# Kernel tuning notes

Hardware: AMD Instinct MI355X
Metric: run time of the kernel (lower is better)

## Reference

```python
import jax, jax.numpy as jnp
import numpy as np
from jax.ops import segment_sum, segment_max

N, E, F, H, G, P, C = 50000, 600000, 128, 128, 64, 32, 10
HEADS = 3
BN_EPS = 1e-5
COS_EPS = 1e-8


def setup_inputs() -> dict:
    key = jax.random.key(0)
    ks = jax.random.split(key, 32)
    rn = lambda k, shape, s: jax.random.normal(k, shape, jnp.float32) * s
    inp = {
        "x": jax.random.normal(ks[0], (N, F), jnp.float32),
        "edge_index": jax.random.randint(ks[1], (2, E), 0, N, jnp.int32),
        "batch": jnp.sort(jax.random.randint(ks[2], (N,), 0, G, jnp.int32)),
        # GCNConv
        "W1": rn(ks[3], (F, H), F ** -0.5), "b1": jnp.zeros((H,), jnp.float32),
        # SAGEConv (lin_l on aggregated neighbors, lin_r on root)
        "Wl": rn(ks[4], (H, H), H ** -0.5), "Wr": rn(ks[5], (H, H), H ** -0.5),
        "bs": jnp.zeros((H,), jnp.float32),
        # GATConv, heads=3, concat=False
        "Wg": rn(ks[6], (H, HEADS * H), H ** -0.5),
        "a_src": rn(ks[7], (HEADS, H), H ** -0.5),
        "a_dst": rn(ks[8], (HEADS, H), H ** -0.5),
        "bg": jnp.zeros((H,), jnp.float32),
        # prototype head / classifier / decoder
        "protos": jax.random.normal(ks[9], (P, H), jnp.float32),
        "Wc": rn(ks[10], (H, C), H ** -0.5), "bc": jnp.zeros((C,), jnp.float32),
        "Wd1": rn(ks[11], (H, 2 * H), H ** -0.5), "bd1": jnp.zeros((2 * H,), jnp.float32),
        "Wd2": rn(ks[12], (2 * H, F), (2 * H) ** -0.5), "bd2": jnp.zeros((F,), jnp.float32),
    }
    # BatchNorm (eval mode): gamma, beta, running mean/var for bn1..bn3
    for i in range(3):
        k0, k1, k2 = jax.random.split(ks[13 + i], 3)
        inp[f"g{i+1}"] = 1.0 + rn(k0, (H,), 0.05)
        inp[f"be{i+1}"] = rn(k1, (H,), 0.05)
        inp[f"m{i+1}"] = rn(k2, (H,), 0.1)
        inp[f"v{i+1}"] = jnp.ones((H,), jnp.float32)
    return inp


def _bn(x, g, b, m, v):
    return (x - m) * jax.lax.rsqrt(v + BN_EPS) * g + b


def _forward(x, edge_index, batch,
             W1, b1, g1, be1, m1, v1,
             Wl, Wr, bs, g2, be2, m2, v2,
             Wg, a_src, a_dst, bg, g3, be3, m3, v3,
             protos, Wc, bc, Wd1, bd1, Wd2, bd2):
    src, dst = edge_index[0], edge_index[1]
    ones_e = jnp.ones((src.shape[0],), x.dtype)

    # --- GCNConv: symmetric norm with self-loops ---
    h = x @ W1                                        # [N, H]
    deg = segment_sum(ones_e, dst, num_segments=N) + 1.0
    dinv = jax.lax.rsqrt(deg)
    coef = dinv[src] * dinv[dst]                      # [E]
    h1 = segment_sum(h[src] * coef[:, None], dst, num_segments=N)
    h1 = h1 + h * (dinv * dinv)[:, None] + b1         # self-loop term + bias
    h1 = jax.nn.elu(_bn(h1, g1, be1, m1, v1))         # dropout = identity (eval)

    # --- SAGEConv: mean aggregation (no self-loops) ---
    cnt = segment_sum(ones_e, dst, num_segments=N)
    mean_nb = segment_sum(h1[src], dst, num_segments=N) / jnp.maximum(cnt, 1.0)[:, None]
    h2 = mean_nb @ Wl + h1 @ Wr + bs
    h2 = jax.nn.elu(_bn(h2, g2, be2, m2, v2))

    # --- GATConv: heads=3, concat=False (mean), with self-loops ---
    hg = (h2 @ Wg).reshape(N, HEADS, H)               # [N, 3, H]
    al_src = jnp.einsum('nhf,hf->nh', hg, a_src)      # [N, 3]
    al_dst = jnp.einsum('nhf,hf->nh', hg, a_dst)
    loop = jnp.arange(N, dtype=src.dtype)
    s2 = jnp.concatenate([src, loop])
    d2 = jnp.concatenate([dst, loop])
    e = jax.nn.leaky_relu(al_src[s2] + al_dst[d2], 0.2)   # [E+N, 3]
    emax = segment_max(e, d2, num_segments=N)             # every node has a self-loop
    ex = jnp.exp(e - emax[d2])
    den = segment_sum(ex, d2, num_segments=N)
    alpha = ex / den[d2]                                  # [E+N, 3]
    h3 = segment_sum(hg[s2] * alpha[:, :, None], d2, num_segments=N)
    h3 = h3.mean(axis=1) + bg                             # concat=False -> head mean
    h3 = jax.nn.elu(_bn(h3, g3, be3, m3, v3))

    # --- global mean pool over graphs ---
    gcnt = segment_sum(jnp.ones((N,), x.dtype), batch, num_segments=G)
    pooled = segment_sum(h3, batch, num_segments=G) / jnp.maximum(gcnt, 1.0)[:, None]

    # --- prototype head: cosine sim -> softmax -> mix ---
    xn = pooled / jnp.maximum(jnp.linalg.norm(pooled, axis=-1, keepdims=True), COS_EPS)
    pn = protos / jnp.maximum(jnp.linalg.norm(protos, axis=-1, keepdims=True), COS_EPS)
    sims = xn @ pn.T                                      # [G, P]
    assignments = jax.nn.softmax(sims, axis=-1)
    proto_emb = assignments @ protos                      # [G, H]
    logits = proto_emb @ Wc + bc                          # [G, C]
    reconstructed = jax.nn.relu(pooled @ Wd1 + bd1) @ Wd2 + bd2   # [G, F]
    return logits, proto_emb, assignments, reconstructed


def reference(x, edge_index, batch,
              W1, b1, g1, be1, m1, v1,
              Wl, Wr, bs, g2, be2, m2, v2,
              Wg, a_src, a_dst, bg, g3, be3, m3, v3,
              protos, Wc, bc, Wd1, bd1, Wd2, bd2):
    return _forward(x, edge_index, batch,
                    W1, b1, g1, be1, m1, v1,
                    Wl, Wr, bs, g2, be2, m2, v2,
                    Wg, a_src, a_dst, bg, g3, be3, m3, v3,
                    protos, Wc, bc, Wd1, bd1, Wd2, bd2)
```

## Files before the change

kernel.cpp:

```cpp
#include <hip/hip_runtime.h>
#include <hip/hip_bf16.h>
#include <stdint.h>
#include <stddef.h>

#define N_ 50000
#define E_ 600000
#define F_ 128
#define H_ 128
#define G_ 64
#define P_ 32
#define C_ 10
#define NB_ 49

typedef __hip_bfloat16 bf16;
typedef __attribute__((ext_vector_type(8))) short short8;
typedef __attribute__((ext_vector_type(4))) float float4v;

__device__ __forceinline__ float b2f(bf16 x){ return __bfloat162float(x); }
__device__ __forceinline__ float us2f(unsigned short u){ return __uint_as_float(((unsigned int)u)<<16); }
__device__ __forceinline__ unsigned short f2us(float x){ bf16 h = __float2bfloat16(x); return *(unsigned short*)&h; }
__device__ __forceinline__ float eluf(float x){ return x>0.f ? x : expm1f(x); }
__device__ __forceinline__ float bnf(float x,float m,float v,float g,float b){ return (x-m)*rsqrtf(v+1e-5f)*g+b; }
__device__ __forceinline__ float lrelu(float x){ return x>0.f ? x : 0.2f*x; }
__device__ __forceinline__ float expc(float x){ return __expf(fminf(x, 50.f)); }
__device__ __forceinline__ void atomAddF(float* a, float v){ unsafeAtomicAdd(a, v); }

__global__ __launch_bounds__(256) void k_wprep(const float* __restrict__ W1, const float* __restrict__ Wl,
    const float* __restrict__ Wr, const float* __restrict__ Wg, unsigned short* __restrict__ WT){
  int idx = blockIdx.x*256 + threadIdx.x;
  if(idx >= 6*16384) return;
  int m = idx >> 14, rem = idx & 16383;
  int n = rem >> 7, k = rem & 127;
  float v;
  if(m==0)      v = W1[k*128+n];
  else if(m==1) v = Wl[k*128+n];
  else if(m==2) v = Wr[k*128+n];
  else          v = Wg[k*384 + (m-3)*128 + n];
  WT[idx] = f2us(v);
}

__device__ __forceinline__ void stage_WT(const unsigned short* __restrict__ WTg, unsigned short* lds, int tid){
  #pragma unroll
  for(int i=0;i<8;i++){
    int idx = tid + i*256;
    int n = idx>>4, c = idx&15;
    uint4 v = *(const uint4*)(WTg + (size_t)idx*8);
    int cs = c ^ (n & 15);
    *(uint4*)(lds + n*128 + cs*8) = v;
  }
}
__device__ __forceinline__ short8 read_Bfrag(const unsigned short* lds, int tile, int kc, int lane){
  int n = tile*16 + (lane&15);
  int c = kc*4 + (lane>>4);
  int cs = c ^ (lane & 15);
  return *(const short8*)(lds + n*128 + cs*8);
}
__device__ __forceinline__ void load_Afrag_bf16(const bf16* A, int row, int lane, short8 af[4]){
  const unsigned short* ap = (const unsigned short*)A + (size_t)row*128 + (lane>>4)*8;
  #pragma unroll
  for(int kc=0;kc<4;kc++) af[kc] = *(const short8*)(ap + kc*32);
}
__device__ __forceinline__ void mfma_pass(const unsigned short* lds, const short8 af[4], int lane, float4v acc[8]){
  #pragma unroll
  for(int tile=0;tile<8;tile++){
    #pragma unroll
    for(int kc=0;kc<4;kc++){
      short8 bfv = read_Bfrag(lds, tile, kc, lane);
      acc[tile] = __builtin_amdgcn_mfma_f32_16x16x32_bf16(af[kc], bfv, acc[tile], 0, 0, 0);
    }
  }
}

__global__ __launch_bounds__(256) void k_mm_x(const float* __restrict__ X, const unsigned short* __restrict__ WTg,
                                              bf16* __restrict__ HB){
  __shared__ unsigned short Wlds[128*128];
  const int tid = threadIdx.x, lane = tid&63, w = tid>>6;
  const int row0 = blockIdx.x*64;
  stage_WT(WTg, Wlds, tid);
  int arow = row0 + w*16 + (lane&15);
  int ar = arow < N_ ? arow : N_-1;
  const float* ap = X + (size_t)ar*128 + (lane>>4)*8;
  short8 af[4];
  #pragma unroll
  for(int kc=0;kc<4;kc++){
    float4 a = *(const float4*)(ap + kc*32);
    float4 b = *(const float4*)(ap + kc*32 + 4);
    short8 v;
    v[0]=(short)f2us(a.x); v[1]=(short)f2us(a.y); v[2]=(short)f2us(a.z); v[3]=(short)f2us(a.w);
    v[4]=(short)f2us(b.x); v[5]=(short)f2us(b.y); v[6]=(short)f2us(b.z); v[7]=(short)f2us(b.w);
    af[kc]=v;
  }
  __syncthreads();
  float4v acc[8];
  #pragma unroll
  for(int t=0;t<8;t++){ acc[t][0]=0.f; acc[t][1]=0.f; acc[t][2]=0.f; acc[t][3]=0.f; }
  mfma_pass(Wlds, af, lane, acc);
  const int colb = lane&15, q = lane>>4;
  unsigned short* ob = (unsigned short*)HB;
  #pragma unroll
  for(int r=0;r<4;r++){
    int ro = row0 + w*16 + q*4 + r;
    if(ro < N_){
      #pragma unroll
      for(int tile=0;tile<8;tile++)
        ob[(size_t)ro*128 + tile*16 + colb] = f2us(acc[tile][r]);
    }
  }
}

__global__ __launch_bounds__(256) void k_sage_mm(const bf16* __restrict__ MaB, const bf16* __restrict__ H1B,
    const unsigned short* __restrict__ WlT, const unsigned short* __restrict__ WrT,
    const float* __restrict__ bs, const float* __restrict__ g2, const float* __restrict__ be2,
    const float* __restrict__ m2, const float* __restrict__ v2, bf16* __restrict__ H2B){
  __shared__ unsigned short Wlds[128*128];
  const int tid = threadIdx.x, lane = tid&63, w = tid>>6;
  const int row0 = blockIdx.x*64;
  int arow = row0 + w*16 + (lane&15);
  int ar = arow < N_ ? arow : N_-1;
  float4v acc[8];
  #pragma unroll
  for(int t=0;t<8;t++){ acc[t][0]=0.f; acc[t][1]=0.f; acc[t][2]=0.f; acc[t][3]=0.f; }
  short8 af[4];

  stage_WT(WlT, Wlds, tid);
  load_Afrag_bf16(MaB, ar, lane, af);
  __syncthreads();
  mfma_pass(Wlds, af, lane, acc);
  __syncthreads();
  stage_WT(WrT, Wlds, tid);
  load_Afrag_bf16(H1B, ar, lane, af);
  __syncthreads();
  mfma_pass(Wlds, af, lane, acc);

  const int colb = lane&15, q = lane>>4;
  unsigned short* ob = (unsigned short*)H2B;
  #pragma unroll
  for(int tile=0;tile<8;tile++){
    int col = tile*16 + colb;
    float bsv=bs[col], gv=g2[col], bev=be2[col], mv=m2[col], vv=v2[col];
    #pragma unroll
    for(int r=0;r<4;r++){
      int ro = row0 + w*16 + q*4 + r;
      if(ro < N_){
        float x = acc[tile][r] + bsv;
        ob[(size_t)ro*128 + col] = f2us(eluf(bnf(x, mv, vv, gv, bev)));
      }
    }
  }
}

__global__ __launch_bounds__(256) void k_gat_mm_all(const bf16* __restrict__ H2B, const unsigned short* __restrict__ WgT,
    const float* __restrict__ a_src, const float* __restrict__ a_dst,
    bf16* __restrict__ HG3, float* __restrict__ als3, float* __restrict__ ald3){
  __shared__ unsigned short Wlds[128*128];
  const int tid = threadIdx.x, lane = tid&63, w = tid>>6;
  const int row0 = blockIdx.x*64;
  int arow = row0 + w*16 + (lane&15);
  int ar = arow < N_ ? arow : N_-1;
  short8 af[4];
  load_Afrag_bf16(H2B, ar, lane, af);
  const int colb = lane&15, q = lane>>4;
  unsigned short* ob = (unsigned short*)HG3;
  for(int hh=0; hh<3; hh++){
    if(hh) __syncthreads();
    stage_WT(WgT + hh*16384, Wlds, tid);
    __syncthreads();
    float4v acc[8];
    #pragma unroll
    for(int t=0;t<8;t++){ acc[t][0]=0.f; acc[t][1]=0.f; acc[t][2]=0.f; acc[t][3]=0.f; }
    mfma_pass(Wlds, af, lane, acc);
    float asv[8], adv[8];
    #pragma unroll
    for(int tile=0;tile<8;tile++){
      asv[tile] = a_src[hh*128 + tile*16 + colb];
      adv[tile] = a_dst[hh*128 + tile*16 + colb];
    }
    #pragma unroll
    for(int r=0;r<4;r++){
      int ro = row0 + w*16 + q*4 + r;
      float ps = 0.f, pd = 0.f;
      #pragma unroll
      for(int tile=0;tile<8;tile++){ ps += acc[tile][r]*asv[tile]; pd += acc[tile][r]*adv[tile]; }
      #pragma unroll
      for(int o=8;o>0;o>>=1){ ps += __shfl_down(ps,o,16); pd += __shfl_down(pd,o,16); }
      if(ro < N_){
        #pragma unroll
        for(int tile=0;tile<8;tile++)
          ob[(size_t)ro*384 + hh*128 + tile*16 + colb] = f2us(acc[tile][r]);
        if(colb == 0){ als3[ro*3+hh] = ps; ald3[ro*3+hh] = pd; }
      }
    }
  }
}

__global__ __launch_bounds__(256) void k_count(const int* __restrict__ dst, int* __restrict__ cnt){
  int e = blockIdx.x*256 + threadIdx.x;
  if(e < E_) atomicAdd(&cnt[dst[e]], 1);
}

__global__ __launch_bounds__(1024) void k_scan1(const int* __restrict__ cnt, int* __restrict__ row_ptr,
                                                float* __restrict__ dinv, int* __restrict__ bsum){
  __shared__ int wsum[16];
  const int t = threadIdx.x, lane = t & 63, wid = t >> 6;
  int i = blockIdx.x*1024 + t;
  int v = (i<N_) ? cnt[i] : 0;
  int x = v;
  #pragma unroll
  for(int o=1;o<64;o<<=1){
    int y = __shfl_up(x, o, 64);
    if(lane >= o) x += y;
  }
  if(lane==63) wsum[wid] = x;
  __syncthreads();
  if(wid==0){
    int s = (lane<16) ? wsum[lane] : 0;
    #pragma unroll
    for(int o=1;o<16;o<<=1){
      int y = __shfl_up(s, o, 64);
      if(lane >= o) s += y;
    }
    if(lane<16) wsum[lane] = s;
  }
  __syncthreads();
  int waveoff = (wid>0) ? wsum[wid-1] : 0;
  int incl = waveoff + x;
  if(i<N_){
    row_ptr[i] = incl - v;
    dinv[i] = rsqrtf((float)v + 1.f);
  }
  if(t==1023) bsum[blockIdx.x] = incl;
}

__global__ __launch_bounds__(64) void k_scan2(const int* __restrict__ bsum, int* __restrict__ boff,
                                              int* __restrict__ row_ptr){
  int lane = threadIdx.x;
  int v = (lane < NB_) ? bsum[lane] : 0;
  int x = v;
  #pragma unroll
  for(int o=1;o<64;o<<=1){
    int y = __shfl_up(x, o, 64);
    if(lane >= o) x += y;
  }
  if(lane < NB_) boff[lane] = x - v;
  if(lane == 63) row_ptr[N_] = x;
}

__global__ __launch_bounds__(256) void k_scan3(int* __restrict__ row_ptr, const int* __restrict__ boff,
                                               int* __restrict__ tmp){
  int i = blockIdx.x*256 + threadIdx.x;
  if(i < N_){
    int r = row_ptr[i] + boff[i>>10];
    row_ptr[i] = r;
    tmp[i] = r;
  }
}

__global__ __launch_bounds__(256) void k_scatter(const int* __restrict__ src, const int* __restrict__ dst,
                                                 int* __restrict__ tmp, int* __restrict__ esrc){
  int e = blockIdx.x*256 + threadIdx.x;
  if(e < E_){
    int d = dst[e];
    int pos = atomicAdd(&tmp[d], 1);
    esrc[pos] = src[e];
  }
}

__global__ __launch_bounds__(256) void k_gcn_gather(const int* __restrict__ row_ptr, const int* __restrict__ esrc,
    const float* __restrict__ dinv, const bf16* __restrict__ HB,
    const float* __restrict__ b1, const float* __restrict__ g1, const float* __restrict__ be1,
    const float* __restrict__ m1, const float* __restrict__ v1, bf16* __restrict__ H1B){
  int n = blockIdx.x*4 + (threadIdx.x>>6);
  int lane = threadIdx.x & 63;
  if(n >= N_) return;
  int beg = row_ptr[n], end = row_ptr[n+1];
  float dn = dinv[n];
  float a0 = 0.f, a1 = 0.f;
  const unsigned short* hb = (const unsigned short*)HB;
  int e = beg;
  for(; e+3 < end; e += 4){
    int s0 = esrc[e], s1 = esrc[e+1], s2 = esrc[e+2], s3 = esrc[e+3];
    unsigned int hv0 = *(const unsigned int*)(hb + (size_t)s0*H_ + lane*2);
    unsigned int hv1 = *(const unsigned int*)(hb + (size_t)s1*H_ + lane*2);
    unsigned int hv2 = *(const unsigned int*)(hb + (size_t)s2*H_ + lane*2);
    unsigned int hv3 = *(const unsigned int*)(hb + (size_t)s3*H_ + lane*2);
    float c0 = dinv[s0]*dn, c1 = dinv[s1]*dn, c2 = dinv[s2]*dn, c3 = dinv[s3]*dn;
    a0 += c0*us2f((unsigned short)(hv0 & 0xFFFFu)) + c1*us2f((unsigned short)(hv1 & 0xFFFFu))
        + c2*us2f((unsigned short)(hv2 & 0xFFFFu)) + c3*us2f((unsigned short)(hv3 & 0xFFFFu));
    a1 += c0*us2f((unsigned short)(hv0 >> 16)) + c1*us2f((unsigned short)(hv1 >> 16))
        + c2*us2f((unsigned short)(hv2 >> 16)) + c3*us2f((unsigned short)(hv3 >> 16));
  }
  for(; e < end; e++){
    int s = esrc[e];
    float c = dinv[s]*dn;
    unsigned int hv = *(const unsigned int*)(hb + (size_t)s*H_ + lane*2);
    a0 += c*us2f((unsigned short)(hv & 0xFFFFu));
    a1 += c*us2f((unsigned short)(hv >> 16));
  }
  unsigned int hv = *(const unsigned int*)(hb + (size_t)n*H_ + lane*2);
  int f0 = lane*2, f1 = f0+1;
  float x0 = a0 + us2f((unsigned short)(hv & 0xFFFFu))*dn*dn + b1[f0];
  float x1 = a1 + us2f((unsigned short)(hv >> 16))*dn*dn + b1[f1];
  x0 = eluf(bnf(x0, m1[f0], v1[f0], g1[f0], be1[f0]));
  x1 = eluf(bnf(x1, m1[f1], v1[f1], g1[f1], be1[f1]));
  unsigned int o = ((unsigned int)f2us(x1)<<16) | f2us(x0);
  *(unsigned int*)((unsigned short*)H1B + (size_t)n*H_ + lane*2) = o;
}

__global__ __launch_bounds__(256) void k_sage_gather(const int* __restrict__ row_ptr, const int* __restrict__ esrc,
    const bf16* __restrict__ H1B, bf16* __restrict__ MeanB){
  int n = blockIdx.x*4 + (threadIdx.x>>6);
  int lane = threadIdx.x & 63;
  if(n >= N_) return;
  int beg = row_ptr[n], end = row_ptr[n+1];
  float a0 = 0.f, a1 = 0.f;
  const unsigned short* hb = (const unsigned short*)H1B;
  int e = beg;
  for(; e+3 < end; e += 4){
    int s0 = esrc[e], s1 = esrc[e+1], s2 = esrc[e+2], s3 = esrc[e+3];
    unsigned int hv0 = *(const unsigned int*)(hb + (size_t)s0*H_ + lane*2);
    unsigned int hv1 = *(const unsigned int*)(hb + (size_t)s1*H_ + lane*2);
    unsigned int hv2 = *(const unsigned int*)(hb + (size_t)s2*H_ + lane*2);
    unsigned int hv3 = *(const unsigned int*)(hb + (size_t)s3*H_ + lane*2);
    a0 += us2f((unsigned short)(hv0 & 0xFFFFu)) + us2f((unsigned short)(hv1 & 0xFFFFu))
        + us2f((unsigned short)(hv2 & 0xFFFFu)) + us2f((unsigned short)(hv3 & 0xFFFFu));
    a1 += us2f((unsigned short)(hv0 >> 16)) + us2f((unsigned short)(hv1 >> 16))
        + us2f((unsigned short)(hv2 >> 16)) + us2f((unsigned short)(hv3 >> 16));
  }
  for(; e < end; e++){
    unsigned int hv = *(const unsigned int*)(hb + (size_t)esrc[e]*H_ + lane*2);
    a0 += us2f((unsigned short)(hv & 0xFFFFu));
    a1 += us2f((unsigned short)(hv >> 16));
  }
  float inv = 1.f / fmaxf((float)(end-beg), 1.f);
  unsigned int o = ((unsigned int)f2us(a1*inv)<<16) | f2us(a0*inv);
  *(unsigned int*)((unsigned short*)MeanB + (size_t)n*H_ + lane*2) = o;
}

__global__ __launch_bounds__(256) void k_gat_gather3(const int* __restrict__ row_ptr, const int* __restrict__ esrc,
    const float* __restrict__ als3, const float* __restrict__ ald3, const bf16* __restrict__ HG3,
    bf16* __restrict__ H3B){
  int n = blockIdx.x*4 + (threadIdx.x>>6);
  int lane = threadIdx.x & 63;
  if(n >= N_) return;
  int beg = row_ptr[n], end = row_ptr[n+1];
  float ald0 = ald3[n*3+0], ald1 = ald3[n*3+1], ald2 = ald3[n*3+2];
  float es0 = expc(lrelu(als3[n*3+0] + ald0));
  float es1 = expc(lrelu(als3[n*3+1] + ald1));
  float es2 = expc(lrelu(als3[n*3+2] + ald2));
  const unsigned short* hb = (const unsigned short*)HG3;
  size_t nb = (size_t)n*384 + lane*2;
  unsigned int h0 = *(const unsigned int*)(hb + nb);
  unsigned int h1 = *(const unsigned int*)(hb + nb + 128);
  unsigned int h2 = *(const unsigned int*)(hb + nb + 256);
  float den0 = es0, den1 = es1, den2 = es2;
  float a00 = es0*us2f((unsigned short)(h0 & 0xFFFFu)), a01 = es0*us2f((unsigned short)(h0 >> 16));
  float a10 = es1*us2f((unsigned short)(h1 & 0xFFFFu)), a11 = es1*us2f((unsigned short)(h1 >> 16));
  float a20 = es2*us2f((unsigned short)(h2 & 0xFFFFu)), a21 = es2*us2f((unsigned short)(h2 >> 16));
  int e = beg;
  for(; e+1 < end; e += 2){
    int s0 = esrc[e], s1 = esrc[e+1];
    size_t b0 = (size_t)s0*384 + lane*2, b1 = (size_t)s1*384 + lane*2;
    unsigned int p00 = *(const unsigned int*)(hb + b0);
    unsigned int p01 = *(const unsigned int*)(hb + b0 + 128);
    unsigned int p02 = *(const unsigned int*)(hb + b0 + 256);
    unsigned int p10 = *(const unsigned int*)(hb + b1);
    unsigned int p11 = *(const unsigned int*)(hb + b1 + 128);
    unsigned int p12 = *(const unsigned int*)(hb + b1 + 256);
    float w00 = expc(lrelu(als3[s0*3+0] + ald0));
    float w01 = expc(lrelu(als3[s0*3+1] + ald1));
    float w02 = expc(lrelu(als3[s0*3+2] + ald2));
    float w10 = expc(lrelu(als3[s1*3+0] + ald0));
    float w11 = expc(lrelu(als3[s1*3+1] + ald1));
    float w12 = expc(lrelu(als3[s1*3+2] + ald2));
    den0 += w00 + w10; den1 += w01 + w11; den2 += w02 + w12;
    a00 += w00*us2f((unsigned short)(p00 & 0xFFFFu)) + w10*us2f((unsigned short)(p10 & 0xFFFFu));
    a01 += w00*us2f((unsigned short)(p00 >> 16))     + w10*us2f((unsigned short)(p10 >> 16));
    a10 += w01*us2f((unsigned short)(p01 & 0xFFFFu)) + w11*us2f((unsigned short)(p11 & 0xFFFFu));
    a11 += w01*us2f((unsigned short)(p01 >> 16))     + w11*us2f((unsigned short)(p11 >> 16));
    a20 += w02*us2f((unsigned short)(p02 & 0xFFFFu)) + w12*us2f((unsigned short)(p12 & 0xFFFFu));
    a21 += w02*us2f((unsigned short)(p02 >> 16))     + w12*us2f((unsigned short)(p12 >> 16));
  }
  if(e < end){
    int s = esrc[e];
    size_t b0 = (size_t)s*384 + lane*2;
    unsigned int p0 = *(const unsigned int*)(hb + b0);
    unsigned int p1 = *(const unsigned int*)(hb + b0 + 128);
    unsigned int p2 = *(const unsigned int*)(hb + b0 + 256);
    float w0 = expc(lrelu(als3[s*3+0] + ald0));
    float w1 = expc(lrelu(als3[s*3+1] + ald1));
    float w2 = expc(lrelu(als3[s*3+2] + ald2));
    den0 += w0; den1 += w1; den2 += w2;
    a00 += w0*us2f((unsigned short)(p0 & 0xFFFFu)); a01 += w0*us2f((unsigned short)(p0 >> 16));
    a10 += w1*us2f((unsigned short)(p1 & 0xFFFFu)); a11 += w1*us2f((unsigned short)(p1 >> 16));
    a20 += w2*us2f((unsigned short)(p2 & 0xFFFFu)); a21 += w2*us2f((unsigned short)(p2 >> 16));
  }
  float i0 = 1.f/(3.f*den0), i1 = 1.f/(3.f*den1), i2 = 1.f/(3.f*den2);
  float r0 = a00*i0 + a10*i1 + a20*i2;
  float r1 = a01*i0 + a11*i1 + a21*i2;
  unsigned int o = ((unsigned int)f2us(r1)<<16) | f2us(r0);
  *(unsigned int*)((unsigned short*)H3B + (size_t)n*H_ + lane*2) = o;
}

#define NPW_ 16
__global__ __launch_bounds__(256) void k_h3fin_pool(const bf16* __restrict__ ACCB, const float* __restrict__ bg,
    const float* __restrict__ g3, const float* __restrict__ be3, const float* __restrict__ m3, const float* __restrict__ v3,
    const int* __restrict__ batch, float* __restrict__ pooled, float* __restrict__ gcnt){
  int wave = blockIdx.x*4 + (threadIdx.x>>6);
  int lane = threadIdx.x & 63;
  int n0 = wave*NPW_;
  if(n0 >= N_) return;
  int n1 = n0 + NPW_; if(n1 > N_) n1 = N_;
  int f0 = lane*2, f1 = f0+1;
  float bg0=bg[f0], bg1=bg[f1];
  float g30=g3[f0], g31=g3[f1], be30=be3[f0], be31=be3[f1];
  float m30=m3[f0], m31=m3[f1], v30=v3[f0], v31=v3[f1];
  float r0=0.f, r1=0.f;
  int cur = batch[n0];
  int seg = 0;
  for(int n=n0; n<n1; n++){
    int b = batch[n];
    if(b != cur){
      atomAddF(&pooled[cur*H_ + f0], r0);
      atomAddF(&pooled[cur*H_ + f1], r1);
      if(lane==0) atomAddF(&gcnt[cur], (float)seg);
      r0 = 0.f; r1 = 0.f; seg = 0; cur = b;
    }
    unsigned int hv = *(const unsigned int*)((const unsigned short*)ACCB + (size_t)n*H_ + lane*2);
    float x0 = us2f((unsigned short)(hv & 0xFFFFu)) + bg0;
    float x1 = us2f((unsigned short)(hv >> 16)) + bg1;
    r0 += eluf(bnf(x0, m30, v30, g30, be30));
    r1 += eluf(bnf(x1, m31, v31, g31, be31));
    seg++;
  }
  atomAddF(&pooled[cur*H_ + f0], r0);
  atomAddF(&pooled[cur*H_ + f1], r1);
  if(lane==0) atomAddF(&gcnt[cur], (float)seg);
}

__global__ __launch_bounds__(128) void k_head(const float* __restrict__ pooledacc, const float* __restrict__ gcnt,
    const float* __restrict__ protos, const float* __restrict__ Wc, const float* __restrict__ bc,
    const float* __restrict__ Wd1, const float* __restrict__ bd1, const float* __restrict__ Wd2, const float* __restrict__ bd2,
    float* __restrict__ out){
  const int g = blockIdx.x, t = threadIdx.x;
  __shared__ float p[128], xn[128], red[128], sims[32], es[32], asg[32], pe[128], t1[256];
  __shared__ float nrm;
  float cg_ = fmaxf(gcnt[g], 1.f);
  p[t] = pooledacc[g*128 + t] / cg_;
  __syncthreads();
  red[t] = p[t]*p[t];
  __syncthreads();
  for(int s=64;s>0;s>>=1){ if(t<s) red[t]+=red[t+s]; __syncthreads(); }
  if(t==0) nrm = fmaxf(sqrtf(red[0]), 1e-8f);
  __syncthreads();
  xn[t] = p[t]/nrm;
  __syncthreads();
  if(t<32){
    float s=0.f, pn=0.f;
    for(int f=0;f<128;f++){ float pv=protos[t*128+f]; s += xn[f]*pv; pn += pv*pv; }
    sims[t] = s / fmaxf(sqrtf(pn), 1e-8f);
  }
  __syncthreads();
  if(t<32){
    float mx=-1e30f;
    for(int j=0;j<32;j++) mx = fmaxf(mx, sims[j]);
    es[t] = __expf(sims[t]-mx);
  }
  __syncthreads();
  if(t<32){
    float sm=0.f;
    for(int j=0;j<32;j++) sm += es[j];
    float a = es[t]/fmaxf(sm,1e-20f);
    asg[t] = a;
    out[8832 + g*32 + t] = a;
  }
  __syncthreads();
  {
    float s=0.f;
    for(int pp=0;pp<32;pp++) s += asg[pp]*protos[pp*128+t];
    pe[t] = s;
    out[640 + g*128 + t] = s;
  }
  __syncthreads();
  if(t<10){
    float s = bc[t];
    for(int f=0;f<128;f++) s += pe[f]*Wc[f*10+t];
    out[g*10 + t] = s;
  }
  for(int j=t;j<256;j+=128){
    float s = bd1[j];
    for(int f=0;f<128;f++) s += p[f]*Wd1[f*256+j];
    t1[j] = fmaxf(s, 0.f);
  }
  __syncthreads();
  {
    float s = bd2[t];
    for(int j=0;j<256;j++) s += t1[j]*Wd2[j*128+t];
    out[10880 + g*128 + t] = s;
  }
}

__global__ void k_sentinel(float* out, float code){
  out[0] = code;
}

extern "C" void kernel_launch(void* const* d_in, const int* in_sizes, int n_in,
                              void* d_out, int out_size, void* d_ws, size_t ws_size,
                              hipStream_t stream){
  const float* X    = (const float*)d_in[0];
  const int*  EI    = (const int*)d_in[1];
  const int*  batch = (const int*)d_in[2];
  const int* src = EI;
  const int* dst = EI + E_;

  int iW1,ib1,iWl,iWr,ibs,iWg,ias,iad,ibg,ipr,iWc,ibc,iWd1,ibd1,iWd2,ibd2;
  int ig1,ibe1,im1,iv1,ig2,ibe2,im2,iv2,ig3,ibe3,im3,iv3;
  if(n_in >= 31 && in_sizes[5] == 128){
    iW1=3; ib1=4; ig1=5; ibe1=6; im1=7; iv1=8;
    iWl=9; iWr=10; ibs=11; ig2=12; ibe2=13; im2=14; iv2=15;
    iWg=16; ias=17; iad=18; ibg=19; ig3=20; ibe3=21; im3=22; iv3=23;
    ipr=24; iWc=25; ibc=26; iWd1=27; ibd1=28; iWd2=29; ibd2=30;
  }else{
    iW1=3; ib1=4; iWl=5; iWr=6; ibs=7; iWg=8; ias=9; iad=10; ibg=11;
    ipr=12; iWc=13; ibc=14; iWd1=15; ibd1=16; iWd2=17; ibd2=18;
    ig1=19; ibe1=20; im1=21; iv1=22; ig2=23; ibe2=24; im2=25; iv2=26;
    ig3=27; ibe3=28; im3=29; iv3=30;
  }
  const float* W1 = (const float*)d_in[iW1];   const float* b1 = (const float*)d_in[ib1];
  const float* Wl = (const float*)d_in[iWl];   const float* Wr = (const float*)d_in[iWr];
  const float* bs = (const float*)d_in[ibs];   const float* Wg = (const float*)d_in[iWg];
  const float* a_src = (const float*)d_in[ias]; const float* a_dst = (const float*)d_in[iad];
  const float* bg = (const float*)d_in[ibg];   const float* protos = (const float*)d_in[ipr];
  const float* Wc = (const float*)d_in[iWc];   const float* bc = (const float*)d_in[ibc];
  const float* Wd1 = (const float*)d_in[iWd1]; const float* bd1 = (const float*)d_in[ibd1];
  const float* Wd2 = (const float*)d_in[iWd2]; const float* bd2 = (const float*)d_in[ibd2];
  const float* g1 = (const float*)d_in[ig1];   const float* be1 = (const float*)d_in[ibe1];
  const float* m1 = (const float*)d_in[im1];   const float* v1 = (const float*)d_in[iv1];
  const float* g2 = (const float*)d_in[ig2];   const float* be2 = (const float*)d_in[ibe2];
  const float* m2 = (const float*)d_in[im2];   const float* v2 = (const float*)d_in[iv2];
  const float* g3 = (const float*)d_in[ig3];   const float* be3 = (const float*)d_in[ibe3];
  const float* m3 = (const float*)d_in[im3];   const float* v3 = (const float*)d_in[iv3];

  const size_t NF = (size_t)N_*H_;
  const size_t intN = (size_t)N_ + (N_+1) + N_ + E_ + 128;
  const size_t fltN = (size_t)6*N_ + G_*H_ + G_;
  const size_t NEED = NF*2*3 + (size_t)N_*384*2 + intN*4 + fltN*4 + (size_t)6*16384*2;
  if(ws_size < NEED){
    k_sentinel<<<1,1,0,stream>>>((float*)d_out, 1000.f + (float)(ws_size>>20));
    return;
  }
  bf16* RA = (bf16*)d_ws;
  bf16* RB = RA + NF;
  bf16* RC = RB + NF;
  bf16* HG3 = RC + NF;
  int*  cnt     = (int*)(HG3 + (size_t)N_*384);
  int*  row_ptr = cnt + N_;
  int*  tmp     = row_ptr + (N_+1);
  int*  esrc    = tmp + N_;
  int*  bsum    = esrc + E_;
  int*  boff    = bsum + 64;
  float* dinv   = (float*)(boff + 64);
  float* als3   = dinv + N_;
  float* ald3   = als3 + (size_t)N_*3;
  float* pooled = ald3 + (size_t)N_*3;
  float* gcnt   = pooled + (size_t)G_*H_;
  unsigned short* WTg = (unsigned short*)(gcnt + G_);

  k_wprep<<<(6*16384+255)/256, 256, 0, stream>>>(W1, Wl, Wr, Wg, WTg);
  hipMemsetAsync(cnt, 0, N_*sizeof(int), stream);
  k_count<<<(E_+255)/256, 256, 0, stream>>>(dst, cnt);
  k_scan1<<<NB_, 1024, 0, stream>>>(cnt, row_ptr, dinv, bsum);
  k_scan2<<<1, 64, 0, stream>>>(bsum, boff, row_ptr);
  k_scan3<<<(N_+255)/256, 256, 0, stream>>>(row_ptr, boff, tmp);
  k_scatter<<<(E_+255)/256, 256, 0, stream>>>(src, dst, tmp, esrc);

  const int GB = (N_+3)/4;
  const int MB = (N_+63)/64;
  k_mm_x<<<MB, 256, 0, stream>>>(X, WTg, RA);
  k_gcn_gather<<<GB, 256, 0, stream>>>(row_ptr, esrc, dinv, RA, b1, g1, be1, m1, v1, RB);
  k_sage_gather<<<GB, 256, 0, stream>>>(row_ptr, esrc, RB, RC);
  k_sage_mm<<<MB, 256, 0, stream>>>(RC, RB, WTg + 16384, WTg + 2*16384, bs, g2, be2, m2, v2, RA);
  k_gat_mm_all<<<MB, 256, 0, stream>>>(RA, WTg + 3*16384, a_src, a_dst, HG3, als3, ald3);
  k_gat_gather3<<<GB, 256, 0, stream>>>(row_ptr, esrc, als3, ald3, HG3, RC);
  hipMemsetAsync(pooled, 0, (size_t)(G_*H_+G_)*sizeof(float), stream);
  {
    int waves = (N_ + NPW_ - 1)/NPW_;
    int blocks = (waves + 3)/4;
    k_h3fin_pool<<<blocks, 256, 0, stream>>>(RC, bg, g3, be3, m3, v3, batch, pooled, gcnt);
  }
  k_head<<<G_, 128, 0, stream>>>(pooled, gcnt, protos, Wc, bc, Wd1, bd1, Wd2, bd2, (float*)d_out);
}
```

Before: 435.2 us.

## Precompute per-edge GCN norms and GAT attention weights in CSR order

The scatter kernel now also stores the destination index and the GCN coefficient dinv[s]*dinv[d] per CSR edge. A new edge-parallel kernel computes the three exponentiated GAT attention logits per edge once, so the gather kernels read contiguous per-edge weights instead of doing random dinv/als3 lookups and exp evaluations on every lane. The aim is to cut redundant transcendental work and scattered scalar loads in the gathers. In exchange it adds an extra kernel launch and several MB of extra edge-array writes and reads.

```diff
diff --git a/kernel.cpp b/kernel.cpp
--- a/kernel.cpp
+++ b/kernel.cpp
@@ -256,17 +256,31 @@
 }
 
 __global__ __launch_bounds__(256) void k_scatter(const int* __restrict__ src, const int* __restrict__ dst,
-                                                 int* __restrict__ tmp, int* __restrict__ esrc){
+    const float* __restrict__ dinv, int* __restrict__ tmp,
+    int* __restrict__ esrc, int* __restrict__ edst, float* __restrict__ cg){
   int e = blockIdx.x*256 + threadIdx.x;
   if(e < E_){
-    int d = dst[e];
+    int s = src[e], d = dst[e];
     int pos = atomicAdd(&tmp[d], 1);
-    esrc[pos] = src[e];
+    esrc[pos] = s;
+    edst[pos] = d;
+    cg[pos] = dinv[s]*dinv[d];
+  }
+}
+
+__global__ __launch_bounds__(256) void k_ew(const int* __restrict__ esrc, const int* __restrict__ edst,
+    const float* __restrict__ als3, const float* __restrict__ ald3, float* __restrict__ ew3){
+  int e = blockIdx.x*256 + threadIdx.x;
+  if(e < E_){
+    int s = esrc[e], d = edst[e];
+    ew3[e*3+0] = expc(lrelu(als3[s*3+0] + ald3[d*3+0]));
+    ew3[e*3+1] = expc(lrelu(als3[s*3+1] + ald3[d*3+1]));
+    ew3[e*3+2] = expc(lrelu(als3[s*3+2] + ald3[d*3+2]));
   }
 }
 
 __global__ __launch_bounds__(256) void k_gcn_gather(const int* __restrict__ row_ptr, const int* __restrict__ esrc,
-    const float* __restrict__ dinv, const bf16* __restrict__ HB,
+    const float* __restrict__ cg, const float* __restrict__ dinv, const bf16* __restrict__ HB,
     const float* __restrict__ b1, const float* __restrict__ g1, const float* __restrict__ be1,
     const float* __restrict__ m1, const float* __restrict__ v1, bf16* __restrict__ H1B){
   int n = blockIdx.x*4 + (threadIdx.x>>6);
@@ -283,7 +297,7 @@
     unsigned int hv1 = *(const unsigned int*)(hb + (size_t)s1*H_ + lane*2);
     unsigned int hv2 = *(const unsigned int*)(hb + (size_t)s2*H_ + lane*2);
     unsigned int hv3 = *(const unsigned int*)(hb + (size_t)s3*H_ + lane*2);
-    float c0 = dinv[s0]*dn, c1 = dinv[s1]*dn, c2 = dinv[s2]*dn, c3 = dinv[s3]*dn;
+    float c0 = cg[e], c1 = cg[e+1], c2 = cg[e+2], c3 = cg[e+3];
     a0 += c0*us2f((unsigned short)(hv0 & 0xFFFFu)) + c1*us2f((unsigned short)(hv1 & 0xFFFFu))
         + c2*us2f((unsigned short)(hv2 & 0xFFFFu)) + c3*us2f((unsigned short)(hv3 & 0xFFFFu));
     a1 += c0*us2f((unsigned short)(hv0 >> 16)) + c1*us2f((unsigned short)(hv1 >> 16))
@@ -291,7 +305,7 @@
   }
   for(; e < end; e++){
     int s = esrc[e];
-    float c = dinv[s]*dn;
+    float c = cg[e];
     unsigned int hv = *(const unsigned int*)(hb + (size_t)s*H_ + lane*2);
     a0 += c*us2f((unsigned short)(hv & 0xFFFFu));
     a1 += c*us2f((unsigned short)(hv >> 16));
@@ -337,16 +351,15 @@
 }
 
 __global__ __launch_bounds__(256) void k_gat_gather3(const int* __restrict__ row_ptr, const int* __restrict__ esrc,
-    const float* __restrict__ als3, const float* __restrict__ ald3, const bf16* __restrict__ HG3,
-    bf16* __restrict__ H3B){
+    const float* __restrict__ ew3, const float* __restrict__ als3, const float* __restrict__ ald3,
+    const bf16* __restrict__ HG3, bf16* __restrict__ H3B){
   int n = blockIdx.x*4 + (threadIdx.x>>6);
   int lane = threadIdx.x & 63;
   if(n >= N_) return;
   int beg = row_ptr[n], end = row_ptr[n+1];
-  float ald0 = ald3[n*3+0], ald1 = ald3[n*3+1], ald2 = ald3[n*3+2];
-  float es0 = expc(lrelu(als3[n*3+0] + ald0));
-  float es1 = expc(lrelu(als3[n*3+1] + ald1));
-  float es2 = expc(lrelu(als3[n*3+2] + ald2));
+  float es0 = expc(lrelu(als3[n*3+0] + ald3[n*3+0]));
+  float es1 = expc(lrelu(als3[n*3+1] + ald3[n*3+1]));
+  float es2 = expc(lrelu(als3[n*3+2] + ald3[n*3+2]));
   const unsigned short* hb = (const unsigned short*)HG3;
   size_t nb = (size_t)n*384 + lane*2;
   unsigned int h0 = *(const unsigned int*)(hb + nb);
@@ -366,12 +379,8 @@
     unsigned int p10 = *(const unsigned int*)(hb + b1);
     unsigned int p11 = *(const unsigned int*)(hb + b1 + 128);
     unsigned int p12 = *(const unsigned int*)(hb + b1 + 256);
-    float w00 = expc(lrelu(als3[s0*3+0] + ald0));
-    float w01 = expc(lrelu(als3[s0*3+1] + ald1));
-    float w02 = expc(lrelu(als3[s0*3+2] + ald2));
-    float w10 = expc(lrelu(als3[s1*3+0] + ald0));
-    float w11 = expc(lrelu(als3[s1*3+1] + ald1));
-    float w12 = expc(lrelu(als3[s1*3+2] + ald2));
+    float w00 = ew3[e*3+0], w01 = ew3[e*3+1], w02 = ew3[e*3+2];
+    float w10 = ew3[e*3+3], w11 = ew3[e*3+4], w12 = ew3[e*3+5];
     den0 += w00 + w10; den1 += w01 + w11; den2 += w02 + w12;
     a00 += w00*us2f((unsigned short)(p00 & 0xFFFFu)) + w10*us2f((unsigned short)(p10 & 0xFFFFu));
     a01 += w00*us2f((unsigned short)(p00 >> 16))     + w10*us2f((unsigned short)(p10 >> 16));
@@ -386,9 +395,7 @@
     unsigned int p0 = *(const unsigned int*)(hb + b0);
     unsigned int p1 = *(const unsigned int*)(hb + b0 + 128);
     unsigned int p2 = *(const unsigned int*)(hb + b0 + 256);
-    float w0 = expc(lrelu(als3[s*3+0] + ald0));
-    float w1 = expc(lrelu(als3[s*3+1] + ald1));
-    float w2 = expc(lrelu(als3[s*3+2] + ald2));
+    float w0 = ew3[e*3+0], w1 = ew3[e*3+1], w2 = ew3[e*3+2];
     den0 += w0; den1 += w1; den2 += w2;
     a00 += w0*us2f((unsigned short)(p0 & 0xFFFFu)); a01 += w0*us2f((unsigned short)(p0 >> 16));
     a10 += w1*us2f((unsigned short)(p1 & 0xFFFFu)); a11 += w1*us2f((unsigned short)(p1 >> 16));
@@ -541,8 +548,8 @@
   const float* m3 = (const float*)d_in[im3];   const float* v3 = (const float*)d_in[iv3];
 
   const size_t NF = (size_t)N_*H_;
-  const size_t intN = (size_t)N_ + (N_+1) + N_ + E_ + 128;
-  const size_t fltN = (size_t)6*N_ + G_*H_ + G_;
+  const size_t intN = (size_t)N_ + (N_+1) + N_ + 2*(size_t)E_ + 128;
+  const size_t fltN = (size_t)E_ + 3*(size_t)E_ + (size_t)7*N_ + G_*H_ + G_;
   const size_t NEED = NF*2*3 + (size_t)N_*384*2 + intN*4 + fltN*4 + (size_t)6*16384*2;
   if(ws_size < NEED){
     k_sentinel<<<1,1,0,stream>>>((float*)d_out, 1000.f + (float)(ws_size>>20));
@@ -556,9 +563,12 @@
   int*  row_ptr = cnt + N_;
   int*  tmp     = row_ptr + (N_+1);
   int*  esrc    = tmp + N_;
-  int*  bsum    = esrc + E_;
+  int*  edst    = esrc + E_;
+  int*  bsum    = edst + E_;
   int*  boff    = bsum + 64;
-  float* dinv   = (float*)(boff + 64);
+  float* cg     = (float*)(boff + 64);
+  float* ew3    = cg + E_;
+  float* dinv   = ew3 + (size_t)3*E_;
   float* als3   = dinv + N_;
   float* ald3   = als3 + (size_t)N_*3;
   float* pooled = ald3 + (size_t)N_*3;
@@ -571,16 +581,17 @@
   k_scan1<<<NB_, 1024, 0, stream>>>(cnt, row_ptr, dinv, bsum);
   k_scan2<<<1, 64, 0, stream>>>(bsum, boff, row_ptr);
   k_scan3<<<(N_+255)/256, 256, 0, stream>>>(row_ptr, boff, tmp);
-  k_scatter<<<(E_+255)/256, 256, 0, stream>>>(src, dst, tmp, esrc);
+  k_scatter<<<(E_+255)/256, 256, 0, stream>>>(src, dst, dinv, tmp, esrc, edst, cg);
 
   const int GB = (N_+3)/4;
   const int MB = (N_+63)/64;
   k_mm_x<<<MB, 256, 0, stream>>>(X, WTg, RA);
-  k_gcn_gather<<<GB, 256, 0, stream>>>(row_ptr, esrc, dinv, RA, b1, g1, be1, m1, v1, RB);
+  k_gcn_gather<<<GB, 256, 0, stream>>>(row_ptr, esrc, cg, dinv, RA, b1, g1, be1, m1, v1, RB);
   k_sage_gather<<<GB, 256, 0, stream>>>(row_ptr, esrc, RB, RC);
   k_sage_mm<<<MB, 256, 0, stream>>>(RC, RB, WTg + 16384, WTg + 2*16384, bs, g2, be2, m2, v2, RA);
   k_gat_mm_all<<<MB, 256, 0, stream>>>(RA, WTg + 3*16384, a_src, a_dst, HG3, als3, ald3);
-  k_gat_gather3<<<GB, 256, 0, stream>>>(row_ptr, esrc, als3, ald3, HG3, RC);
+  k_ew<<<(E_+255)/256, 256, 0, stream>>>(esrc, edst, als3, ald3, ew3);
+  k_gat_gather3<<<GB, 256, 0, stream>>>(row_ptr, esrc, ew3, als3, ald3, HG3, RC);
   hipMemsetAsync(pooled, 0, (size_t)(G_*H_+G_)*sizeof(float), stream);
   {
     int waves = (N_ + NPW_ - 1)/NPW_;
```

Result: slower. 444.0 us (+2.0%).
